# Performance work log

Hardware: AMD Instinct MI355X
Metric: run time of the kernel (lower is better)

The kernel has to match this reference:

```python
import jax, jax.numpy as jnp
import numpy as np

B, S, E = 2, 2048, 1024
H = 16
A = 1024
DH = A // H  # 64 per-head attention dim


def setup_inputs() -> dict:
    key = jax.random.key(0)
    ks = jax.random.split(key, 9)
    s = lambda fan_in: 1.0 / np.sqrt(fan_in)
    return {
        "x": jax.random.normal(ks[0], (B, S, E), dtype=jnp.float32),
        # per-head Q/K/V projections stacked over heads: [H, E, DH]
        "Wq": jax.random.normal(ks[1], (H, E, DH), dtype=jnp.float32) * s(E),
        "bq": jnp.zeros((H, DH), dtype=jnp.float32),
        "Wk": jax.random.normal(ks[2], (H, E, DH), dtype=jnp.float32) * s(E),
        "bk": jnp.zeros((H, DH), dtype=jnp.float32),
        "Wv": jax.random.normal(ks[3], (H, E, DH), dtype=jnp.float32) * s(E),
        "bv": jnp.zeros((H, DH), dtype=jnp.float32),
        # output projection Linear(A, E): stored as [A, E]
        "Wo": jax.random.normal(ks[4], (A, E), dtype=jnp.float32) * s(A),
        "bo": jnp.zeros((E,), dtype=jnp.float32),
    }


def reference(x, Wq, bq, Wk, bk, Wv, bv, Wo, bo):
    # Batched equivalent of the per-head Python loop:
    # each head: q = x Wq_h + bq_h ; scores = q k^T / sqrt(DH) ; softmax ; @ v
    q = jnp.einsum("bse,hed->bhsd", x, Wq) + bq[None, :, None, :]
    k = jnp.einsum("bse,hed->bhsd", x, Wk) + bk[None, :, None, :]
    v = jnp.einsum("bse,hed->bhsd", x, Wv) + bv[None, :, None, :]
    scale = 1.0 / jnp.sqrt(jnp.asarray(DH, dtype=x.dtype))
    scores = jnp.einsum("bhsd,bhtd->bhst", q, k) * scale  # [B,H,S,S]
    attn = jax.nn.softmax(scores, axis=-1)
    heads = jnp.einsum("bhst,bhtd->bhsd", attn, v)  # [B,H,S,DH]
    # concat heads along last dim (matches torch.cat over head outputs)
    concat = heads.transpose(0, 2, 1, 3).reshape(x.shape[0], x.shape[1], H * DH)
    return concat @ Wo + bo  # final Linear(dim_attention, dim_embedding)
```

## Files before the change

kernel.cpp:

```cpp
#include <hip/hip_runtime.h>
#include <math.h>


namespace {
constexpr int kBn = 2, kS = 2048, kE = 1024, kH = 16, kDH = 64, kA = 1024;

typedef __attribute__((ext_vector_type(8))) short short8;
typedef __attribute__((ext_vector_type(4))) float f32x4;

#define QSCALE 0.18033688011112042f

__device__ inline unsigned short f2bf(float f) {
  union { float f; unsigned u; } x; x.f = f;
  unsigned r = x.u + 0x7fffu + ((x.u >> 16) & 1u);
  return (unsigned short)(r >> 16);
}

__device__ inline void gld16(const void* g, void* l) {
  __builtin_amdgcn_global_load_lds(
      (const __attribute__((address_space(1))) unsigned int*)g,
      (__attribute__((address_space(3))) unsigned int*)l, 16, 0, 0);
}

__device__ inline void lds_barrier() {
  asm volatile("s_waitcnt lgkmcnt(0)" ::: "memory");
  __builtin_amdgcn_s_barrier();
}

__global__ __launch_bounds__(256) void cast_x_kernel(
    const float* __restrict__ x, unsigned short* __restrict__ xb) {
  const int i = (blockIdx.x * 256 + threadIdx.x) * 8;
  float4 a = *(const float4*)(x + i);
  float4 b = *(const float4*)(x + i + 4);
  unsigned short t[8];
  t[0] = f2bf(a.x); t[1] = f2bf(a.y); t[2] = f2bf(a.z); t[3] = f2bf(a.w);
  t[4] = f2bf(b.x); t[5] = f2bf(b.y); t[6] = f2bf(b.z); t[7] = f2bf(b.w);
  *(short8*)(xb + i) = *(const short8*)t;
}

__global__ __launch_bounds__(256) void cast_wqkv_kernel(
    const float* __restrict__ Wq, const float* __restrict__ Wk,
    const float* __restrict__ Wv, unsigned short* __restrict__ Wt) {
  const int sel = blockIdx.z;
  const float* __restrict__ W = (sel == 0) ? Wq : (sel == 1) ? Wk : Wv;
  const int h = blockIdx.y;
  const int e0 = blockIdx.x * 64;
  const int tid = threadIdx.x;

  __shared__ float T[64][68];
  const int el = tid >> 2, dq = tid & 3;
  const float* src = W + ((size_t)h * kE + e0 + el) * kDH + dq * 16;
#pragma unroll
  for (int j = 0; j < 4; ++j)
    *(float4*)&T[el][dq * 16 + j * 4] = *(const float4*)(src + j * 4);
  __syncthreads();

  const int d = tid & 63, w = tid >> 6;
  unsigned short t[16];
#pragma unroll
  for (int j = 0; j < 16; ++j) t[j] = f2bf(T[w * 16 + j][d]);
  unsigned short* dst =
      Wt + (((size_t)sel << 20) | ((size_t)(h * 64 + d) << 10)) + e0 + w * 16;
  *(short8*)dst = *(const short8*)&t[0];
  *(short8*)(dst + 8) = *(const short8*)&t[8];
}

__global__ __launch_bounds__(256) void cast_wo_kernel(
    const float* __restrict__ Wo, unsigned short* __restrict__ Wot) {
  const int a0 = blockIdx.x * 64, e0 = blockIdx.y * 64;
  const int tid = threadIdx.x;

  __shared__ float T[64][68];
  const int al = tid >> 2, dq = tid & 3;
  const float* src = Wo + (size_t)(a0 + al) * kE + e0 + dq * 16;
#pragma unroll
  for (int j = 0; j < 4; ++j)
    *(float4*)&T[al][dq * 16 + j * 4] = *(const float4*)(src + j * 4);
  __syncthreads();

  const int e = tid & 63, w = tid >> 6;
  unsigned short t[16];
#pragma unroll
  for (int j = 0; j < 16; ++j) t[j] = f2bf(T[w * 16 + j][e]);
  unsigned short* dst = Wot + ((size_t)(e0 + e) << 10) + a0 + w * 16;
  *(short8*)dst = *(const short8*)&t[0];
  *(short8*)(dst + 8) = *(const short8*)&t[8];
}

__global__ __launch_bounds__(256) void gemm_bf16_kernel(
    const unsigned short* __restrict__ A, const unsigned short* __restrict__ Bt,
    const float* __restrict__ b0, const float* __restrict__ b1,
    const float* __restrict__ b2,
    unsigned short* __restrict__ oq, unsigned short* __restrict__ okk,
    unsigned short* __restrict__ ov) {
  constexpr int K = 1024;
  const int mode = (int)blockIdx.z;
  const unsigned short* Bm = Bt + ((size_t)blockIdx.z << 20);
  const float* bias = (mode == 1) ? b1 : (mode == 2) ? b2 : b0;

  const int mt = blockIdx.x, nt = blockIdx.y;
  const int tid = threadIdx.x;
  const int wv = tid >> 6, lane = tid & 63, lq = lane & 15, quad = lane >> 4;
  const int wm = wv >> 1, wn = wv & 1;

  __shared__ unsigned short lA[128 * 32];
  __shared__ unsigned short lB[128 * 32];

  const int c0 = wv * 64 + lane;
  const int c1 = c0 + 256;
  const unsigned short* gA0 = A + (size_t)(mt * 128 + (c0 >> 2)) * K + (c0 & 3) * 8;
  const unsigned short* gA1 = A + (size_t)(mt * 128 + (c1 >> 2)) * K + (c1 & 3) * 8;
  const unsigned short* gB0 = Bm + (size_t)(nt * 128 + (c0 >> 2)) * K + (c0 & 3) * 8;
  const unsigned short* gB1 = Bm + (size_t)(nt * 128 + (c1 >> 2)) * K + (c1 & 3) * 8;
  unsigned short* lA0 = lA + (size_t)(wv * 64) * 8;
  unsigned short* lA1 = lA0 + 256 * 8;
  unsigned short* lB0 = lB + (size_t)(wv * 64) * 8;
  unsigned short* lB1 = lB0 + 256 * 8;

  f32x4 acc[4][4];
#pragma unroll
  for (int i = 0; i < 4; ++i)
#pragma unroll
    for (int j = 0; j < 4; ++j) acc[i][j] = (f32x4){0.f, 0.f, 0.f, 0.f};

  for (int k0 = 0; k0 < K; k0 += 32) {
    gld16(gA0 + k0, lA0);
    gld16(gA1 + k0, lA1);
    gld16(gB0 + k0, lB0);
    gld16(gB1 + k0, lB1);
    __syncthreads();
    short8 af[4], bfr[4];
#pragma unroll
    for (int i = 0; i < 4; ++i)
      af[i] = *(const short8*)&lA[(wm * 64 + i * 16 + lq) * 32 + quad * 8];
#pragma unroll
    for (int j = 0; j < 4; ++j)
      bfr[j] = *(const short8*)&lB[(wn * 64 + j * 16 + lq) * 32 + quad * 8];
#pragma unroll
    for (int i = 0; i < 4; ++i)
#pragma unroll
      for (int j = 0; j < 4; ++j)
        acc[i][j] = __builtin_amdgcn_mfma_f32_16x16x32_bf16(af[i], bfr[j],
                                                            acc[i][j], 0, 0, 0);
    __syncthreads();
  }

  const int n0 = nt * 128 + wn * 64;
  float bv4[4];
#pragma unroll
  for (int j = 0; j < 4; ++j) bv4[j] = bias[n0 + j * 16 + lq];

  const int tok0 = mt * 128 + wm * 64;
  const int b = tok0 >> 11;
  const int s0 = tok0 & (kS - 1);
  const int h = n0 >> 6;
  if (mode < 2) {
    unsigned short* o = (mode == 0) ? oq : okk;
    const float scl = (mode == 0) ? QSCALE : 1.0f;
#pragma unroll
    for (int i = 0; i < 4; ++i)
#pragma unroll
      for (int j = 0; j < 4; ++j) {
        const int d = j * 16 + lq;
#pragma unroll
        for (int r = 0; r < 4; ++r) {
          const int s = s0 + i * 16 + quad * 4 + r;
          o[((size_t)(b * kH + h) * kS + s) * kDH + d] =
              f2bf((acc[i][j][r] + bv4[j]) * scl);
        }
      }
  } else {
#pragma unroll
    for (int i = 0; i < 4; ++i)
#pragma unroll
      for (int j = 0; j < 4; ++j) {
        const int d = j * 16 + lq;
        union { unsigned short u[4]; uint2 v; } pk;
#pragma unroll
        for (int r = 0; r < 4; ++r) pk.u[r] = f2bf(acc[i][j][r] + bv4[j]);
        const int s = s0 + i * 16 + quad * 4;
        *(uint2*)(ov + ((size_t)(b * kH + h) * kDH + d) * kS + s) = pk.v;
      }
  }
}

__global__ __launch_bounds__(256) void gemm_out_kernel(
    const unsigned short* __restrict__ A, const unsigned short* __restrict__ Bt,
    const float* __restrict__ bo, float* __restrict__ of) {
  constexpr int K = 1024;
  const int mt = blockIdx.x, nt = blockIdx.y;
  const int tid = threadIdx.x;
  const int wv = tid >> 6, lane = tid & 63, lq = lane & 15, quad = lane >> 4;
  const int wm = wv >> 1, wn = wv & 1;

  __shared__ unsigned short lA[128 * 32];
  __shared__ unsigned short lB[64 * 32];

  const int c0 = wv * 64 + lane;
  const int c1 = c0 + 256;
  const unsigned short* gA0 = A + (size_t)(mt * 128 + (c0 >> 2)) * K + (c0 & 3) * 8;
  const unsigned short* gA1 = A + (size_t)(mt * 128 + (c1 >> 2)) * K + (c1 & 3) * 8;
  const unsigned short* gB0 = Bt + (size_t)(nt * 64 + (c0 >> 2)) * K + (c0 & 3) * 8;
  unsigned short* lA0 = lA + (size_t)(wv * 64) * 8;
  unsigned short* lA1 = lA0 + 256 * 8;
  unsigned short* lB0 = lB + (size_t)(wv * 64) * 8;

  f32x4 acc[4][2];
#pragma unroll
  for (int i = 0; i < 4; ++i)
#pragma unroll
    for (int j = 0; j < 2; ++j) acc[i][j] = (f32x4){0.f, 0.f, 0.f, 0.f};

  for (int k0 = 0; k0 < K; k0 += 32) {
    gld16(gA0 + k0, lA0);
    gld16(gA1 + k0, lA1);
    gld16(gB0 + k0, lB0);
    __syncthreads();
    short8 af[4], bfr[2];
#pragma unroll
    for (int i = 0; i < 4; ++i)
      af[i] = *(const short8*)&lA[(wm * 64 + i * 16 + lq) * 32 + quad * 8];
#pragma unroll
    for (int j = 0; j < 2; ++j)
      bfr[j] = *(const short8*)&lB[(wn * 32 + j * 16 + lq) * 32 + quad * 8];
#pragma unroll
    for (int i = 0; i < 4; ++i)
#pragma unroll
      for (int j = 0; j < 2; ++j)
        acc[i][j] = __builtin_amdgcn_mfma_f32_16x16x32_bf16(af[i], bfr[j],
                                                            acc[i][j], 0, 0, 0);
    __syncthreads();
  }

  const int n0 = nt * 64 + wn * 32;
  const int m0 = mt * 128 + wm * 64;
  float bv2[2];
#pragma unroll
  for (int j = 0; j < 2; ++j) bv2[j] = bo[n0 + j * 16 + lq];
#pragma unroll
  for (int i = 0; i < 4; ++i)
#pragma unroll
    for (int j = 0; j < 2; ++j)
#pragma unroll
      for (int r = 0; r < 4; ++r)
        of[(size_t)(m0 + i * 16 + quad * 4 + r) * kE + n0 + j * 16 + lq] =
            acc[i][j][r] + bv2[j];
}

#define QT 128
#define KT 64
#define LDK 72
__global__ __launch_bounds__(256) void attn_mfma_kernel(
    const unsigned short* __restrict__ q, const unsigned short* __restrict__ k,
    const unsigned short* __restrict__ vt, unsigned short* __restrict__ cc) {
  const int bh = blockIdx.y;
  const int b = bh >> 4, h = bh & 15;
  const int tid = threadIdx.x;
  const int wv = tid >> 6;
  const int lane = tid & 63;
  const int lq = lane & 15;
  const int quad = lane >> 4;

  __shared__ unsigned short Ks[KT][LDK];
  __shared__ unsigned short Vt[kDH][LDK];
  __shared__ unsigned short Pb[QT][LDK];

  const int q0 = blockIdx.x * QT;

  short8 qa[2][2];
#pragma unroll
  for (int mf = 0; mf < 2; ++mf) {
    const unsigned short* qbase =
        q + ((size_t)bh * kS + q0 + wv * 32 + mf * 16 + lq) * kDH;
    qa[mf][0] = *(const short8*)(qbase + quad * 8);
    qa[mf][1] = *(const short8*)(qbase + 32 + quad * 8);
  }

  f32x4 Oacc[2][4];
  f32x4 Osum[2];
#pragma unroll
  for (int mf = 0; mf < 2; ++mf) {
    Osum[mf] = (f32x4){0.f, 0.f, 0.f, 0.f};
#pragma unroll
    for (int dt = 0; dt < 4; ++dt) Oacc[mf][dt] = (f32x4){0.f, 0.f, 0.f, 0.f};
  }

  unsigned short ob[8];
#pragma unroll
  for (int i = 0; i < 8; ++i) ob[i] = 0x3F80;
  const short8 ones = *(const short8*)ob;

  const unsigned short* kg = k + (size_t)bh * kS * kDH;
  const unsigned short* vg = vt + (size_t)bh * kDH * kS;

  const int sr = tid >> 3;
  const int sc = (tid & 7) << 3;

  short8 rk0 = *(const short8*)(kg + (size_t)sr * kDH + sc);
  short8 rk1 = *(const short8*)(kg + (size_t)(sr + 32) * kDH + sc);
  short8 rv0 = *(const short8*)(vg + (size_t)sr * kS + sc);
  short8 rv1 = *(const short8*)(vg + (size_t)(sr + 32) * kS + sc);

  for (int t0 = 0; t0 < kS; t0 += KT) {
    lds_barrier();
    *(short8*)&Ks[sr][sc]       = rk0;
    *(short8*)&Ks[sr + 32][sc]  = rk1;
    *(short8*)&Vt[sr][sc]       = rv0;
    *(short8*)&Vt[sr + 32][sc]  = rv1;
    if (t0 + KT < kS) {
      const int tn = t0 + KT;
      rk0 = *(const short8*)(kg + (size_t)(tn + sr) * kDH + sc);
      rk1 = *(const short8*)(kg + (size_t)(tn + sr + 32) * kDH + sc);
      rv0 = *(const short8*)(vg + (size_t)sr * kS + tn + sc);
      rv1 = *(const short8*)(vg + (size_t)(sr + 32) * kS + tn + sc);
    }
    lds_barrier();

    f32x4 S[2][4];
#pragma unroll
    for (int nt = 0; nt < 4; ++nt) {
      short8 kb0 = *(const short8*)&Ks[nt * 16 + lq][quad * 8];
      short8 kb1 = *(const short8*)&Ks[nt * 16 + lq][32 + quad * 8];
#pragma unroll
      for (int mf = 0; mf < 2; ++mf) {
        f32x4 acc = (f32x4){0.f, 0.f, 0.f, 0.f};
        acc = __builtin_amdgcn_mfma_f32_16x16x32_bf16(qa[mf][0], kb0, acc, 0, 0, 0);
        acc = __builtin_amdgcn_mfma_f32_16x16x32_bf16(qa[mf][1], kb1, acc, 0, 0, 0);
        S[mf][nt] = acc;
      }
    }

#pragma unroll
    for (int mf = 0; mf < 2; ++mf)
#pragma unroll
      for (int nt = 0; nt < 4; ++nt)
#pragma unroll
        for (int r = 0; r < 4; ++r) {
          const float p = __builtin_amdgcn_exp2f(S[mf][nt][r]);
          union { float f; unsigned u; } x; x.f = p;
          Pb[wv * 32 + mf * 16 + quad * 4 + r][nt * 16 + lq] =
              (unsigned short)((x.u + 0x8000u) >> 16);
        }

    short8 pa[2][2];
#pragma unroll
    for (int mf = 0; mf < 2; ++mf) {
      pa[mf][0] = *(const short8*)&Pb[wv * 32 + mf * 16 + lq][quad * 8];
      pa[mf][1] = *(const short8*)&Pb[wv * 32 + mf * 16 + lq][32 + quad * 8];
    }

#pragma unroll
    for (int dt = 0; dt < 4; ++dt) {
      short8 vb0 = *(const short8*)&Vt[dt * 16 + lq][quad * 8];
      short8 vb1 = *(const short8*)&Vt[dt * 16 + lq][32 + quad * 8];
#pragma unroll
      for (int mf = 0; mf < 2; ++mf) {
        Oacc[mf][dt] =
            __builtin_amdgcn_mfma_f32_16x16x32_bf16(pa[mf][0], vb0, Oacc[mf][dt], 0, 0, 0);
        Oacc[mf][dt] =
            __builtin_amdgcn_mfma_f32_16x16x32_bf16(pa[mf][1], vb1, Oacc[mf][dt], 0, 0, 0);
      }
    }
#pragma unroll
    for (int mf = 0; mf < 2; ++mf) {
      Osum[mf] = __builtin_amdgcn_mfma_f32_16x16x32_bf16(pa[mf][0], ones, Osum[mf], 0, 0, 0);
      Osum[mf] = __builtin_amdgcn_mfma_f32_16x16x32_bf16(pa[mf][1], ones, Osum[mf], 0, 0, 0);
    }
  }

#pragma unroll
  for (int mf = 0; mf < 2; ++mf)
#pragma unroll
    for (int r = 0; r < 4; ++r) {
      const float inv = 1.0f / Osum[mf][r];
      const int qrow = q0 + wv * 32 + mf * 16 + quad * 4 + r;
      unsigned short* base = cc + ((size_t)b * kS + qrow) * kA + h * kDH;
#pragma unroll
      for (int dt = 0; dt < 4; ++dt)
        base[dt * 16 + lq] = f2bf(Oacc[mf][dt][r] * inv);
    }
}

}

extern "C" void kernel_launch(void* const* d_in, const int* in_sizes, int n_in,
                              void* d_out, int out_size, void* d_ws, size_t ws_size,
                              hipStream_t stream) {
  const float* x  = (const float*)d_in[0];
  const float* Wq = (const float*)d_in[1];
  const float* bq = (const float*)d_in[2];
  const float* Wk = (const float*)d_in[3];
  const float* bk = (const float*)d_in[4];
  const float* Wv = (const float*)d_in[5];
  const float* bv = (const float*)d_in[6];
  const float* Wo = (const float*)d_in[7];
  const float* bo = (const float*)d_in[8];
  float* out = (float*)d_out;

  const size_t per = (size_t)kBn * kH * kS * kDH;
  unsigned short* xb  = (unsigned short*)d_ws;
  unsigned short* qb  = xb + per;
  unsigned short* kb  = qb + per;
  unsigned short* vtb = kb + per;
  unsigned short* cc  = vtb + per;
  unsigned short* Wt  = cc + per;
  unsigned short* Wot = Wt + 3 * (per / 4);

  cast_x_kernel<<<dim3(per / (256 * 8)), 256, 0, stream>>>(x, xb);
  cast_wqkv_kernel<<<dim3(16, 16, 3), 256, 0, stream>>>(Wq, Wk, Wv, Wt);
  cast_wo_kernel<<<dim3(16, 16), 256, 0, stream>>>(Wo, Wot);

  gemm_bf16_kernel<<<dim3(32, 8, 3), 256, 0, stream>>>(
      xb, Wt, bq, bk, bv, qb, kb, vtb);

  attn_mfma_kernel<<<dim3(kS / QT, kBn * kH), 256, 0, stream>>>(qb, kb, vtb, cc);

  gemm_out_kernel<<<dim3(32, 16), 256, 0, stream>>>(cc, Wot, bo, out);
}
```

Measured before the change: 197.7 us.

## Compute transposed scores with 16x16x16 MFMA to keep P in registers

Computes S^T = K·Q^T using 16x16x16 bf16 MFMA so that the softmax probabilities come out in the exact register layout needed as the B operand for the P·V and row-sum MFMAs. This removes the shared-memory round trip for P (the Pb buffer and its stores and loads) and shrinks LDS use. In exchange it issues twice as many MFMA instructions of half the K-depth, which have lower throughput per instruction than the 16x16x32 variant on CDNA3/4. The old path is kept as a fallback when the builtin is unavailable.

```diff
diff --git a/kernel.cpp b/kernel.cpp
--- a/kernel.cpp
+++ b/kernel.cpp
@@ -6,7 +6,18 @@
 constexpr int kBn = 2, kS = 2048, kE = 1024, kH = 16, kDH = 64, kA = 1024;
 
 typedef __attribute__((ext_vector_type(8))) short short8;
+typedef __attribute__((ext_vector_type(4))) short short4;
 typedef __attribute__((ext_vector_type(4))) float f32x4;
+
+#if __has_builtin(__builtin_amdgcn_mfma_f32_16x16x16_bf16_1k)
+#define HAVE_MFMA16 1
+#define MFMA16(a, b, c) __builtin_amdgcn_mfma_f32_16x16x16_bf16_1k(a, b, c, 0, 0, 0)
+#elif __has_builtin(__builtin_amdgcn_mfma_f32_16x16x16_bf16)
+#define HAVE_MFMA16 1
+#define MFMA16(a, b, c) __builtin_amdgcn_mfma_f32_16x16x16_bf16(a, b, c, 0, 0, 0)
+#else
+#define HAVE_MFMA16 0
+#endif
 
 #define QSCALE 0.18033688011112042f
 
@@ -263,32 +274,11 @@
 
   __shared__ unsigned short Ks[KT][LDK];
   __shared__ unsigned short Vt[kDH][LDK];
+#if !HAVE_MFMA16
   __shared__ unsigned short Pb[QT][LDK];
+#endif
 
   const int q0 = blockIdx.x * QT;
-
-  short8 qa[2][2];
-#pragma unroll
-  for (int mf = 0; mf < 2; ++mf) {
-    const unsigned short* qbase =
-        q + ((size_t)bh * kS + q0 + wv * 32 + mf * 16 + lq) * kDH;
-    qa[mf][0] = *(const short8*)(qbase + quad * 8);
-    qa[mf][1] = *(const short8*)(qbase + 32 + quad * 8);
-  }
-
-  f32x4 Oacc[2][4];
-  f32x4 Osum[2];
-#pragma unroll
-  for (int mf = 0; mf < 2; ++mf) {
-    Osum[mf] = (f32x4){0.f, 0.f, 0.f, 0.f};
-#pragma unroll
-    for (int dt = 0; dt < 4; ++dt) Oacc[mf][dt] = (f32x4){0.f, 0.f, 0.f, 0.f};
-  }
-
-  unsigned short ob[8];
-#pragma unroll
-  for (int i = 0; i < 8; ++i) ob[i] = 0x3F80;
-  const short8 ones = *(const short8*)ob;
 
   const unsigned short* kg = k + (size_t)bh * kS * kDH;
   const unsigned short* vg = vt + (size_t)bh * kDH * kS;
@@ -301,12 +291,37 @@
   short8 rv0 = *(const short8*)(vg + (size_t)sr * kS + sc);
   short8 rv1 = *(const short8*)(vg + (size_t)(sr + 32) * kS + sc);
 
+#if HAVE_MFMA16
+  short4 qb16[2][4];
+#pragma unroll
+  for (int mf = 0; mf < 2; ++mf) {
+    const unsigned short* qbase =
+        q + ((size_t)bh * kS + q0 + wv * 32 + mf * 16 + lq) * kDH;
+#pragma unroll
+    for (int c = 0; c < 4; ++c)
+      qb16[mf][c] = *(const short4*)(qbase + c * 16 + quad * 4);
+  }
+
+  unsigned short o4[4];
+#pragma unroll
+  for (int i = 0; i < 4; ++i) o4[i] = 0x3F80;
+  const short4 ones4 = *(const short4*)o4;
+
+  f32x4 OaccT[4][2];
+  f32x4 Osum[2];
+#pragma unroll
+  for (int mf = 0; mf < 2; ++mf) {
+    Osum[mf] = (f32x4){0.f, 0.f, 0.f, 0.f};
+#pragma unroll
+    for (int dt = 0; dt < 4; ++dt) OaccT[dt][mf] = (f32x4){0.f, 0.f, 0.f, 0.f};
+  }
+
   for (int t0 = 0; t0 < kS; t0 += KT) {
     lds_barrier();
-    *(short8*)&Ks[sr][sc]       = rk0;
-    *(short8*)&Ks[sr + 32][sc]  = rk1;
-    *(short8*)&Vt[sr][sc]       = rv0;
-    *(short8*)&Vt[sr + 32][sc]  = rv1;
+    *(short8*)&Ks[sr][sc]      = rk0;
+    *(short8*)&Ks[sr + 32][sc] = rk1;
+    *(short8*)&Vt[sr][sc]      = rv0;
+    *(short8*)&Vt[sr + 32][sc] = rv1;
     if (t0 + KT < kS) {
       const int tn = t0 + KT;
       rk0 = *(const short8*)(kg + (size_t)(tn + sr) * kDH + sc);
@@ -316,6 +331,109 @@
     }
     lds_barrier();
 
+    f32x4 ST[4][2];
+#pragma unroll
+    for (int tt = 0; tt < 4; ++tt) {
+      short4 ak[4];
+#pragma unroll
+      for (int c = 0; c < 4; ++c)
+        ak[c] = *(const short4*)&Ks[tt * 16 + lq][c * 16 + quad * 4];
+#pragma unroll
+      for (int mf = 0; mf < 2; ++mf) {
+        f32x4 a = (f32x4){0.f, 0.f, 0.f, 0.f};
+#pragma unroll
+        for (int c = 0; c < 4; ++c) a = MFMA16(ak[c], qb16[mf][c], a);
+        ST[tt][mf] = a;
+      }
+    }
+
+    short4 pp[4][2];
+#pragma unroll
+    for (int tt = 0; tt < 4; ++tt)
+#pragma unroll
+      for (int mf = 0; mf < 2; ++mf) {
+        union { unsigned short u[4]; short4 v; } pk;
+#pragma unroll
+        for (int r = 0; r < 4; ++r) {
+          const float p = __builtin_amdgcn_exp2f(ST[tt][mf][r]);
+          union { float f; unsigned u; } x; x.f = p;
+          pk.u[r] = (unsigned short)((x.u + 0x8000u) >> 16);
+        }
+        pp[tt][mf] = pk.v;
+      }
+
+#pragma unroll
+    for (int mf = 0; mf < 2; ++mf)
+#pragma unroll
+      for (int tt = 0; tt < 4; ++tt)
+        Osum[mf] = MFMA16(ones4, pp[tt][mf], Osum[mf]);
+
+#pragma unroll
+    for (int dt = 0; dt < 4; ++dt) {
+      short4 av[4];
+#pragma unroll
+      for (int tt = 0; tt < 4; ++tt)
+        av[tt] = *(const short4*)&Vt[dt * 16 + lq][tt * 16 + quad * 4];
+#pragma unroll
+      for (int mf = 0; mf < 2; ++mf)
+#pragma unroll
+        for (int tt = 0; tt < 4; ++tt)
+          OaccT[dt][mf] = MFMA16(av[tt], pp[tt][mf], OaccT[dt][mf]);
+    }
+  }
+
+#pragma unroll
+  for (int mf = 0; mf < 2; ++mf) {
+    const float inv = 1.0f / Osum[mf][0];
+    const int qrow = q0 + wv * 32 + mf * 16 + lq;
+    unsigned short* base = cc + ((size_t)b * kS + qrow) * kA + h * kDH;
+#pragma unroll
+    for (int dt = 0; dt < 4; ++dt) {
+      union { unsigned short u[4]; uint2 v; } o;
+#pragma unroll
+      for (int r = 0; r < 4; ++r) o.u[r] = f2bf(OaccT[dt][mf][r] * inv);
+      *(uint2*)(base + dt * 16 + quad * 4) = o.v;
+    }
+  }
+#else
+  short8 qa[2][2];
+#pragma unroll
+  for (int mf = 0; mf < 2; ++mf) {
+    const unsigned short* qbase =
+        q + ((size_t)bh * kS + q0 + wv * 32 + mf * 16 + lq) * kDH;
+    qa[mf][0] = *(const short8*)(qbase + quad * 8);
+    qa[mf][1] = *(const short8*)(qbase + 32 + quad * 8);
+  }
+
+  f32x4 Oacc[2][4];
+  f32x4 Osum[2];
+#pragma unroll
+  for (int mf = 0; mf < 2; ++mf) {
+    Osum[mf] = (f32x4){0.f, 0.f, 0.f, 0.f};
+#pragma unroll
+    for (int dt = 0; dt < 4; ++dt) Oacc[mf][dt] = (f32x4){0.f, 0.f, 0.f, 0.f};
+  }
+
+  unsigned short ob[8];
+#pragma unroll
+  for (int i = 0; i < 8; ++i) ob[i] = 0x3F80;
+  const short8 ones = *(const short8*)ob;
+
+  for (int t0 = 0; t0 < kS; t0 += KT) {
+    lds_barrier();
+    *(short8*)&Ks[sr][sc]      = rk0;
+    *(short8*)&Ks[sr + 32][sc] = rk1;
+    *(short8*)&Vt[sr][sc]      = rv0;
+    *(short8*)&Vt[sr + 32][sc] = rv1;
+    if (t0 + KT < kS) {
+      const int tn = t0 + KT;
+      rk0 = *(const short8*)(kg + (size_t)(tn + sr) * kDH + sc);
+      rk1 = *(const short8*)(kg + (size_t)(tn + sr + 32) * kDH + sc);
+      rv0 = *(const short8*)(vg + (size_t)sr * kS + tn + sc);
+      rv1 = *(const short8*)(vg + (size_t)(sr + 32) * kS + tn + sc);
+    }
+    lds_barrier();
+
     f32x4 S[2][4];
 #pragma unroll
     for (int nt = 0; nt < 4; ++nt) {
@@ -323,10 +441,10 @@
       short8 kb1 = *(const short8*)&Ks[nt * 16 + lq][32 + quad * 8];
 #pragma unroll
       for (int mf = 0; mf < 2; ++mf) {
-        f32x4 acc = (f32x4){0.f, 0.f, 0.f, 0.f};
-        acc = __builtin_amdgcn_mfma_f32_16x16x32_bf16(qa[mf][0], kb0, acc, 0, 0, 0);
-        acc = __builtin_amdgcn_mfma_f32_16x16x32_bf16(qa[mf][1], kb1, acc, 0, 0, 0);
-        S[mf][nt] = acc;
+        f32x4 a = (f32x4){0.f, 0.f, 0.f, 0.f};
+        a = __builtin_amdgcn_mfma_f32_16x16x32_bf16(qa[mf][0], kb0, a, 0, 0, 0);
+        a = __builtin_amdgcn_mfma_f32_16x16x32_bf16(qa[mf][1], kb1, a, 0, 0, 0);
+        S[mf][nt] = a;
       }
     }
 
@@ -379,6 +497,7 @@
       for (int dt = 0; dt < 4; ++dt)
         base[dt * 16 + lq] = f2bf(Oacc[mf][dt][r] * inv);
     }
+#endif
 }
 
 }
```

New measurement: 203.3 us. +2.8%, slower.
